# Optimization experiments

Measured on AMD Instinct MI355X. Metric: run time of the kernel, lower is better.

## Reference

```python
import jax, jax.numpy as jnp
import numpy as np

G, S, D, H, E = 8, 2048, 1024, 4096, 8  # groups, group_size, d_model, ffn_hidden, experts


def setup_inputs() -> dict:
    key = jax.random.key(0)
    ks = jax.random.split(key, 6)
    s = 0.02
    return {
        "x": jax.random.normal(ks[0], (G, S, D), dtype=jnp.float32),
        "gate_w": jax.random.normal(ks[1], (D, E), dtype=jnp.float32) * s,
        "ew1": jax.random.normal(ks[2], (E, D, H), dtype=jnp.float32) * s,
        "eb1": jnp.zeros((E, H), dtype=jnp.float32),
        "ew2": jax.random.normal(ks[3], (E, H, D), dtype=jnp.float32) * s,
        "eb2": jnp.zeros((E, D), dtype=jnp.float32),
        "sw1": jax.random.normal(ks[4], (D, H), dtype=jnp.float32) * s,
        "sb1": jnp.zeros((H,), dtype=jnp.float32),
        "sw2": jax.random.normal(ks[5], (H, D), dtype=jnp.float32) * s,
        "sb2": jnp.zeros((D,), dtype=jnp.float32),
        "expert_capacity": 2048,
    }


def reference(x, gate_w, ew1, eb1, ew2, eb2, sw1, sb1, sw2, sb2, expert_capacity):
    g, s_, d = x.shape
    e = gate_w.shape[1]
    T = g * s_
    cap = int(expert_capacity)

    # ---- Router (inference path) ----
    router_logits = jnp.einsum('gsd,de->gse', x, gate_w)           # (G,S,E)
    router_probs = jax.nn.softmax(router_logits, axis=-1)
    flat_probs = router_probs.transpose(2, 0, 1).reshape(e, T)      # (E,T)
    pad_w = max(0, cap - T)
    if pad_w > 0:
        flat_probs = jnp.pad(flat_probs, ((0, 0), (0, pad_w)),
                             mode='constant', constant_values=-1e9)
    scores, token_indices = jax.lax.top_k(flat_probs, k=cap)        # (E,C)
    scores = jnp.where(scores > -1e8, scores, 0.0)

    # ---- Routed experts: gather -> grouped FFN -> scale -> scatter-add ----
    x_flat = x.reshape(T, d)                                        # (T,D)
    safe_idx = jnp.clip(token_indices, 0, T - 1)                    # guard padded slots
    toks = x_flat[safe_idx]                                         # (E,C,D)
    h = jax.nn.gelu(jnp.einsum('ecd,edh->ech', toks, ew1) + eb1[:, None, :])
    y = jnp.einsum('ech,ehd->ecd', h, ew2) + eb2[:, None, :]        # (E,C,D)
    y = y * scores[..., None]                                       # zero weight kills padded slots
    routed = jnp.zeros_like(x_flat).at[safe_idx.reshape(-1)].add(y.reshape(-1, d))

    # ---- Shared expert over all tokens ----
    shared = jax.nn.gelu(x_flat @ sw1 + sb1) @ sw2 + sb2            # (T,D)

    return (routed + shared).reshape(g, s_, d)
```

## Files before the change

### kernel.cpp

```cpp
#include <hip/hip_runtime.h>

typedef __bf16 bf16;
typedef __bf16 bf16x8 __attribute__((ext_vector_type(8)));
typedef float f32x4 __attribute__((ext_vector_type(4)));

#define NTOK 16384
#define DMODEL 1024
#define HFFN 4096
#define NEXP 8
#define CAP 2048

#define VMCNT(n) asm volatile("s_waitcnt vmcnt(" #n ")" ::: "memory")
#define LGKM0() do { asm volatile("s_waitcnt lgkmcnt(0)" ::: "memory"); \
                     __builtin_amdgcn_sched_barrier(0); } while (0)
#define RAWBAR() do { __builtin_amdgcn_sched_barrier(0); \
                      __builtin_amdgcn_s_barrier(); \
                      __builtin_amdgcn_sched_barrier(0); } while (0)

__device__ __forceinline__ void gload16(const void* g, void* l) {
  __builtin_amdgcn_global_load_lds((const __attribute__((address_space(1))) void*)g,
                                   (__attribute__((address_space(3))) void*)l, 16, 0, 0);
}

__device__ __forceinline__ float gelu_f(float v) {
  float u = 0.7978845608028654f * (v + 0.044715f * v * v * v);
  float ex = __expf(2.0f * u);
  float th = 1.0f - 2.0f / (ex + 1.0f);
  return 0.5f * v * (1.0f + th);
}

__device__ __forceinline__ void xcd_remap(int& bx, int& by) {
  const int gx = gridDim.x;
  const int lg = 31 - __clz((unsigned)gx);
  const int w = blockIdx.x + gx * blockIdx.y;
  bx = (w >> 3) & (gx - 1);
  by = (w & 7) | (((w >> 3) >> lg) << 3);
}

__global__ __launch_bounds__(256) void cvt_x_kernel(const float* __restrict__ x,
                                                    bf16* __restrict__ xb) {
  int i = blockIdx.x * blockDim.x + threadIdx.x;
  const float4* a = (const float4*)x + (size_t)i * 2;
  float4 v0 = a[0], v1 = a[1];
  bf16x8 o;
  o[0]=(bf16)v0.x; o[1]=(bf16)v0.y; o[2]=(bf16)v0.z; o[3]=(bf16)v0.w;
  o[4]=(bf16)v1.x; o[5]=(bf16)v1.y; o[6]=(bf16)v1.z; o[7]=(bf16)v1.w;
  *(bf16x8*)(xb + (size_t)i * 8) = o;
}

__global__ __launch_bounds__(64) void router_kernel(const float* __restrict__ x,
                                                    const float* __restrict__ gw,
                                                    float* __restrict__ probs) {
  int t = blockIdx.x;
  int l = threadIdx.x;
  int e = l & 7, chunk = l >> 3;
  const float* xr = x + (size_t)t * DMODEL + chunk * 128;
  const float* gwr = gw + (size_t)(chunk * 128) * NEXP + e;
  float a0 = 0.f, a1 = 0.f;
  #pragma unroll
  for (int d = 0; d < 128; d += 8) {
    float4 xv = *(const float4*)(xr + d);
    float4 xw = *(const float4*)(xr + d + 4);
    a0 += xv.x * gwr[(d+0)*8] + xv.y * gwr[(d+1)*8] + xv.z * gwr[(d+2)*8] + xv.w * gwr[(d+3)*8];
    a1 += xw.x * gwr[(d+4)*8] + xw.y * gwr[(d+5)*8] + xw.z * gwr[(d+6)*8] + xw.w * gwr[(d+7)*8];
  }
  float acc = a0 + a1;
  acc += __shfl_xor(acc, 8);
  acc += __shfl_xor(acc, 16);
  acc += __shfl_xor(acc, 32);
  float m = acc;
  m = fmaxf(m, __shfl_xor(m, 1));
  m = fmaxf(m, __shfl_xor(m, 2));
  m = fmaxf(m, __shfl_xor(m, 4));
  float ex = expf(acc - m);
  float s = ex;
  s += __shfl_xor(s, 1); s += __shfl_xor(s, 2); s += __shfl_xor(s, 4);
  if (l < 8) probs[(size_t)e * NTOK + t] = ex / s;
}

__global__ __launch_bounds__(256) void topk_kernel(const float* __restrict__ probs,
                                                   int* __restrict__ oidx,
                                                   float* __restrict__ oscr) {
  const int e = blockIdx.x;
  const float* p = probs + (size_t)e * NTOK;
  const int t = threadIdx.x;
  __shared__ unsigned hist[256];
  __shared__ unsigned sg[256], sq[256];
  __shared__ unsigned bcast[4];
  unsigned pref = 0, krem = CAP;
  for (int pass = 0; pass < 4; ++pass) {
    const int sh = 24 - pass * 8;
    hist[t] = 0;
    __syncthreads();
    for (int j = 0; j < 64; ++j) {
      unsigned u = __float_as_uint(p[t * 64 + j]);
      bool ok = (pass == 0) || ((u >> (sh + 8)) == pref);
      if (ok) atomicAdd(&hist[(u >> sh) & 255u], 1u);
    }
    __syncthreads();
    if (t == 0) {
      unsigned cum = 0; int b = 255;
      for (; b > 0; --b) {
        unsigned c = hist[b];
        if (cum + c >= krem) break;
        cum += c;
      }
      bcast[0] = (pref << 8) | (unsigned)b;
      bcast[1] = krem - cum;
    }
    __syncthreads();
    pref = bcast[0];
    krem = bcast[1];
  }
  const unsigned thr = pref;
  const unsigned neq_take = krem;
  unsigned cgt = 0, ceq = 0;
  for (int j = 0; j < 64; ++j) {
    unsigned u = __float_as_uint(p[t * 64 + j]);
    cgt += (u > thr);
    ceq += (u == thr);
  }
  sg[t] = cgt; sq[t] = ceq;
  __syncthreads();
  if (t == 0) {
    unsigned ag = 0, aq = 0;
    for (int i = 0; i < 256; ++i) {
      unsigned g = sg[i], q = sq[i];
      sg[i] = ag; sq[i] = aq;
      ag += g; aq += q;
    }
    bcast[2] = ag;
  }
  __syncthreads();
  const unsigned ngt = bcast[2];
  unsigned og = sg[t], oq = sq[t];
  int* oi = oidx + e * CAP;
  float* os = oscr + e * CAP;
  for (int j = 0; j < 64; ++j) {
    int tok = t * 64 + j;
    float pv = p[tok];
    unsigned u = __float_as_uint(pv);
    if (u > thr) {
      oi[og] = tok; os[og] = pv; ++og;
    } else if (u == thr) {
      if (oq < neq_take) { oi[ngt + oq] = tok; os[ngt + oq] = pv; }
      ++oq;
    }
  }
}

__global__ __launch_bounds__(256) void transpose_cvt(const float* __restrict__ in_e,
                                                     const float* __restrict__ in_s,
                                                     bf16* __restrict__ outp,
                                                     int R, int C) {
  int z = blockIdx.z;
  const float* in = (z < 8) ? (in_e + (size_t)z * (size_t)R * C) : in_s;
  bf16* out = outp + (size_t)z * (size_t)R * C;
  __shared__ float tile[64][65];
  int tx = threadIdx.x & 63, ty = threadIdx.x >> 6;
  int c0 = blockIdx.x * 64, r0 = blockIdx.y * 64;
  #pragma unroll
  for (int j = 0; j < 16; ++j) {
    int r = ty + j * 4;
    tile[r][tx] = in[(size_t)(r0 + r) * C + c0 + tx];
  }
  __syncthreads();
  #pragma unroll
  for (int j = 0; j < 16; ++j) {
    int c = ty + j * 4;
    out[(size_t)(c0 + c) * R + r0 + tx] = (bf16)tile[tx][c];
  }
}


#define STAGE_TILE_ALL(tt) do { \
  bf16* D_ = smem + (((tt) & 1) << 15); \
  const int ko_ = (tt) * 64; \
  gload16(srcA0 + ko_, D_ + tid8); \
  gload16(srcA1 + ko_, D_ + 4096 + tid8); \
  gload16(srcA2 + ko_, D_ + 8192 + tid8); \
  gload16(srcA3 + ko_, D_ + 12288 + tid8); \
  gload16(srcB0 + ko_, D_ + 16384 + tid8); \
  gload16(srcB1 + ko_, D_ + 20480 + tid8); \
  gload16(srcB2 + ko_, D_ + 24576 + tid8); \
  gload16(srcB3 + ko_, D_ + 28672 + tid8); \
} while (0)

#define KLOOP8(NT) do { \
  STAGE_TILE_ALL(0); \
  STAGE_TILE_ALL(1); \
  VMCNT(8); \
  RAWBAR(); \
  for (int t = 0; t < (NT); ++t) { \
    const bf16* Ab_ = smem + ((t & 1) << 15); \
    const bf16* Bb_ = Ab_ + 16384; \
    bf16* Sn_ = smem + ((t & 1) << 15); \
    const int ko2 = (t + 2) * 64; \
    const bool st = (t + 2) < (NT); \
    bf16x8 aA[8], aB[8]; \
     \
    _Pragma("unroll") for (int i = 0; i < 4; ++i) { \
      aA[i*2+0] = *(const bf16x8*)(Ab_ + (wr*128 + i*16 + fr)*64 + c0s); \
      aA[i*2+1] = *(const bf16x8*)(Ab_ + (wr*128 + i*16 + fr)*64 + c1s); \
    } \
    _Pragma("unroll") for (int j = 0; j < 2; ++j) { \
      aB[j*2+0] = *(const bf16x8*)(Bb_ + (wc*64 + j*16 + fr)*64 + c0s); \
      aB[j*2+1] = *(const bf16x8*)(Bb_ + (wc*64 + j*16 + fr)*64 + c1s); \
    } \
    RAWBAR(); LGKM0(); \
    __builtin_amdgcn_s_setprio(1); \
    _Pragma("unroll") for (int i = 0; i < 4; ++i) \
      _Pragma("unroll") for (int j = 0; j < 2; ++j) { \
        acc[i][j] = __builtin_amdgcn_mfma_f32_16x16x32_bf16(aA[i*2+0], aB[j*2+0], acc[i][j], 0, 0, 0); \
        acc[i][j] = __builtin_amdgcn_mfma_f32_16x16x32_bf16(aA[i*2+1], aB[j*2+1], acc[i][j], 0, 0, 0); \
      } \
    __builtin_amdgcn_s_setprio(0); \
    RAWBAR(); \
     \
    _Pragma("unroll") for (int j = 0; j < 2; ++j) { \
      aB[4+j*2+0] = *(const bf16x8*)(Bb_ + (wc*64 + 32 + j*16 + fr)*64 + c0s); \
      aB[4+j*2+1] = *(const bf16x8*)(Bb_ + (wc*64 + 32 + j*16 + fr)*64 + c1s); \
    } \
    if (st) { \
      gload16(srcA0 + ko2, Sn_ + tid8); \
      gload16(srcA2 + ko2, Sn_ + 8192 + tid8); \
    } \
    RAWBAR(); LGKM0(); \
    __builtin_amdgcn_s_setprio(1); \
    _Pragma("unroll") for (int i = 0; i < 4; ++i) \
      _Pragma("unroll") for (int j = 0; j < 2; ++j) { \
        acc[i][2+j] = __builtin_amdgcn_mfma_f32_16x16x32_bf16(aA[i*2+0], aB[4+j*2+0], acc[i][2+j], 0, 0, 0); \
        acc[i][2+j] = __builtin_amdgcn_mfma_f32_16x16x32_bf16(aA[i*2+1], aB[4+j*2+1], acc[i][2+j], 0, 0, 0); \
      } \
    __builtin_amdgcn_s_setprio(0); \
    RAWBAR(); \
     \
    _Pragma("unroll") for (int i = 0; i < 4; ++i) { \
      aA[i*2+0] = *(const bf16x8*)(Ab_ + (wr*128 + 64 + i*16 + fr)*64 + c0s); \
      aA[i*2+1] = *(const bf16x8*)(Ab_ + (wr*128 + 64 + i*16 + fr)*64 + c1s); \
    } \
    if (st) { \
      gload16(srcB0 + ko2, Sn_ + 16384 + tid8); \
      gload16(srcB1 + ko2, Sn_ + 20480 + tid8); \
      gload16(srcB2 + ko2, Sn_ + 24576 + tid8); \
      gload16(srcB3 + ko2, Sn_ + 28672 + tid8); \
    } \
    RAWBAR(); LGKM0(); \
    __builtin_amdgcn_s_setprio(1); \
    _Pragma("unroll") for (int i = 0; i < 4; ++i) \
      _Pragma("unroll") for (int j = 0; j < 2; ++j) { \
        acc[4+i][j] = __builtin_amdgcn_mfma_f32_16x16x32_bf16(aA[i*2+0], aB[j*2+0], acc[4+i][j], 0, 0, 0); \
        acc[4+i][j] = __builtin_amdgcn_mfma_f32_16x16x32_bf16(aA[i*2+1], aB[j*2+1], acc[4+i][j], 0, 0, 0); \
      } \
    __builtin_amdgcn_s_setprio(0); \
    RAWBAR(); \
     \
    if (st) { \
      gload16(srcA1 + ko2, Sn_ + 4096 + tid8); \
      gload16(srcA3 + ko2, Sn_ + 12288 + tid8); \
    } \
    __builtin_amdgcn_s_setprio(1); \
    _Pragma("unroll") for (int i = 0; i < 4; ++i) \
      _Pragma("unroll") for (int j = 0; j < 2; ++j) { \
        acc[4+i][2+j] = __builtin_amdgcn_mfma_f32_16x16x32_bf16(aA[i*2+0], aB[4+j*2+0], acc[4+i][2+j], 0, 0, 0); \
        acc[4+i][2+j] = __builtin_amdgcn_mfma_f32_16x16x32_bf16(aA[i*2+1], aB[4+j*2+1], acc[4+i][2+j], 0, 0, 0); \
      } \
    __builtin_amdgcn_s_setprio(0); \
    if (st) { VMCNT(8); } else { VMCNT(0); } \
    RAWBAR(); \
  } \
} while (0)

__global__ __launch_bounds__(512, 2) void ffn1_gemm(const bf16* __restrict__ xb,
                                                    const bf16* __restrict__ w1t,
                                                    const float* __restrict__ bias1,
                                                    const int* __restrict__ sel,
                                                    bf16* __restrict__ hout,
                                                    int routed) {
  const int e = blockIdx.z;
  const bf16* Bw = w1t + (routed ? (size_t)e * HFFN * DMODEL : 0);
  const float* bias = bias1 + (routed ? (size_t)e * HFFN : 0);
  bf16* hb = hout + (routed ? (size_t)e * CAP * HFFN : 0);
  int bx, by;
  xcd_remap(bx, by);
  const int m0 = by * 256, n0 = bx * 256;
  __shared__ __align__(16) bf16 smem[65536];
  const int tid = threadIdx.x, lane = tid & 63, wave = tid >> 6;
  const int wr = wave >> 2, wc = wave & 3;
  const int tid8 = tid * 8;

  const int srow = tid >> 3, sch = tid & 7;
  const int schs = sch ^ (srow & 7);
  const bf16 *srcA0, *srcA1, *srcA2, *srcA3, *srcB0, *srcB1, *srcB2, *srcB3;
  {
    int ra0 = routed ? sel[e * CAP + m0 + srow]       : (m0 + srow);
    int ra1 = routed ? sel[e * CAP + m0 + 64 + srow]  : (m0 + 64 + srow);
    int ra2 = routed ? sel[e * CAP + m0 + 128 + srow] : (m0 + 128 + srow);
    int ra3 = routed ? sel[e * CAP + m0 + 192 + srow] : (m0 + 192 + srow);
    srcA0 = xb + (size_t)ra0 * DMODEL + schs * 8;
    srcA1 = xb + (size_t)ra1 * DMODEL + schs * 8;
    srcA2 = xb + (size_t)ra2 * DMODEL + schs * 8;
    srcA3 = xb + (size_t)ra3 * DMODEL + schs * 8;
    srcB0 = Bw + (size_t)(n0 + srow) * DMODEL + schs * 8;
    srcB1 = Bw + (size_t)(n0 + 64 + srow) * DMODEL + schs * 8;
    srcB2 = Bw + (size_t)(n0 + 128 + srow) * DMODEL + schs * 8;
    srcB3 = Bw + (size_t)(n0 + 192 + srow) * DMODEL + schs * 8;
  }

  f32x4 acc[8][4];
  #pragma unroll
  for (int i = 0; i < 8; ++i)
    #pragma unroll
    for (int j = 0; j < 4; ++j) acc[i][j] = (f32x4){0.f, 0.f, 0.f, 0.f};

  const int fr = lane & 15;
  const int k8 = lane >> 4;
  const int sw = lane & 7;
  const int c0s = (k8 ^ sw) * 8;
  const int c1s = ((k8 + 4) ^ sw) * 8;

  KLOOP8(DMODEL / 64);

  #pragma unroll
  for (int half = 0; half < 2; ++half) {
    if (wr == half) {
      #pragma unroll
      for (int i = 0; i < 8; ++i) {
        #pragma unroll
        for (int j = 0; j < 4; ++j) {
          const int nl = wc * 64 + j * 16 + fr;
          const float bb = bias[n0 + nl];
          #pragma unroll
          for (int q = 0; q < 4; ++q) {
            const int ml = i * 16 + (lane >> 4) * 4 + q;
            smem[ml * 256 + (nl ^ (((ml >> 2) & 7) << 4))] =
                (bf16)gelu_f(acc[i][j][q] + bb);
          }
        }
      }
    }
    __syncthreads();
    #pragma unroll
    for (int p = 0; p < 8; ++p) {
      const int flat = p * 512 + tid;
      const int row = flat >> 5, nc8 = flat & 31;
      uint4 v = *(const uint4*)(smem + row * 256 + ((nc8 * 8) ^ (((row >> 2) & 7) << 4)));
      *(uint4*)(hb + (size_t)(m0 + half * 128 + row) * HFFN + n0 + nc8 * 8) = v;
    }
    __syncthreads();
  }
}

__global__ __launch_bounds__(512, 2) void ffn2_gemm(const bf16* __restrict__ hbuf,
                                                    const bf16* __restrict__ w2t,
                                                    const float* __restrict__ bias2,
                                                    const int* __restrict__ sel,
                                                    const float* __restrict__ scr,
                                                    float* __restrict__ out,
                                                    int routed) {
  const int e = blockIdx.z;
  const bf16* Ab = hbuf + (routed ? (size_t)e * CAP * HFFN : 0);
  const bf16* Bw = w2t + (routed ? (size_t)e * DMODEL * HFFN : 0);
  const float* bias = bias2 + (routed ? (size_t)e * DMODEL : 0);
  int bx, by;
  xcd_remap(bx, by);
  const int m0 = by * 256, n0 = bx * 256;
  __shared__ __align__(16) bf16 smem[65536];
  __shared__ int s_tok[256];
  __shared__ float s_scl[256];
  const int tid = threadIdx.x, lane = tid & 63, wave = tid >> 6;
  const int wr = wave >> 2, wc = wave & 3;
  const int tid8 = tid * 8;

  const int srow = tid >> 3, sch = tid & 7;
  const int schs = sch ^ (srow & 7);
  const bf16* srcA0 = Ab + (size_t)(m0 + srow) * HFFN + schs * 8;
  const bf16* srcA1 = Ab + (size_t)(m0 + 64 + srow) * HFFN + schs * 8;
  const bf16* srcA2 = Ab + (size_t)(m0 + 128 + srow) * HFFN + schs * 8;
  const bf16* srcA3 = Ab + (size_t)(m0 + 192 + srow) * HFFN + schs * 8;
  const bf16* srcB0 = Bw + (size_t)(n0 + srow) * HFFN + schs * 8;
  const bf16* srcB1 = Bw + (size_t)(n0 + 64 + srow) * HFFN + schs * 8;
  const bf16* srcB2 = Bw + (size_t)(n0 + 128 + srow) * HFFN + schs * 8;
  const bf16* srcB3 = Bw + (size_t)(n0 + 192 + srow) * HFFN + schs * 8;
  if (routed && tid < 256) {
    s_tok[tid] = sel[e * CAP + m0 + tid];
    s_scl[tid] = scr[e * CAP + m0 + tid];
  }

  f32x4 acc[8][4];
  #pragma unroll
  for (int i = 0; i < 8; ++i)
    #pragma unroll
    for (int j = 0; j < 4; ++j) acc[i][j] = (f32x4){0.f, 0.f, 0.f, 0.f};

  const int fr = lane & 15;
  const int k8 = lane >> 4;
  const int sw = lane & 7;
  const int c0s = (k8 ^ sw) * 8;
  const int c1s = ((k8 + 4) ^ sw) * 8;

  KLOOP8(HFFN / 64);

  if (!routed) {
    #pragma unroll
    for (int i = 0; i < 8; ++i) {
      #pragma unroll
      for (int j = 0; j < 4; ++j) {
        const int nl = wc * 64 + j * 16 + fr;
        const float bb = bias[n0 + nl];
        #pragma unroll
        for (int q = 0; q < 4; ++q) {
          const int ml = wr * 128 + i * 16 + (lane >> 4) * 4 + q;
          out[(size_t)(m0 + ml) * DMODEL + n0 + nl] = acc[i][j][q] + bb;
        }
      }
    }
  } else {
    __syncthreads();
    #pragma unroll
    for (int i = 0; i < 8; ++i) {
      #pragma unroll
      for (int j = 0; j < 4; ++j) {
        const int nl = wc * 64 + j * 16 + fr;
        const float bb = bias[n0 + nl];
        #pragma unroll
        for (int q = 0; q < 4; ++q) {
          const int ml = wr * 128 + i * 16 + (lane >> 4) * 4 + q;
          const int tok = s_tok[ml];
          const float sc = s_scl[ml];
          atomicAdd(out + (size_t)tok * DMODEL + n0 + nl, (acc[i][j][q] + bb) * sc);
        }
      }
    }
  }
}

extern "C" void kernel_launch(void* const* d_in, const int* in_sizes, int n_in,
                              void* d_out, int out_size, void* d_ws, size_t ws_size,
                              hipStream_t stream) {
  const float* x   = (const float*)d_in[0];
  const float* gw  = (const float*)d_in[1];
  const float* ew1 = (const float*)d_in[2];
  const float* eb1 = (const float*)d_in[3];
  const float* ew2 = (const float*)d_in[4];
  const float* eb2 = (const float*)d_in[5];
  const float* sw1 = (const float*)d_in[6];
  const float* sb1 = (const float*)d_in[7];
  const float* sw2 = (const float*)d_in[8];
  const float* sb2 = (const float*)d_in[9];
  float* out = (float*)d_out;

  char* ws = (char*)d_ws;
  size_t off = 0;
  bf16* xb      = (bf16*)(ws + off); off += (size_t)NTOK * DMODEL * 2;
  bf16* w1t     = (bf16*)(ws + off); off += (size_t)9 * HFFN * DMODEL * 2;
  bf16* w2t     = (bf16*)(ws + off); off += (size_t)9 * DMODEL * HFFN * 2;
  bf16* hbuf    = (bf16*)(ws + off); off += (size_t)NTOK * HFFN * 2;
  float* probs  = (float*)(ws + off); off += (size_t)NEXP * NTOK * 4;
  int* selidx   = (int*)(ws + off);   off += (size_t)NEXP * CAP * 4;
  float* selscr = (float*)(ws + off); off += (size_t)NEXP * CAP * 4;

  cvt_x_kernel<<<dim3(NTOK * DMODEL / 8 / 256), dim3(256), 0, stream>>>(x, xb);
  router_kernel<<<dim3(NTOK), dim3(64), 0, stream>>>(x, gw, probs);
  topk_kernel<<<dim3(NEXP), dim3(256), 0, stream>>>(probs, selidx, selscr);
  transpose_cvt<<<dim3(HFFN / 64, DMODEL / 64, 9), dim3(256), 0, stream>>>(ew1, sw1, w1t, DMODEL, HFFN);
  transpose_cvt<<<dim3(DMODEL / 64, HFFN / 64, 9), dim3(256), 0, stream>>>(ew2, sw2, w2t, HFFN, DMODEL);

  ffn1_gemm<<<dim3(HFFN / 256, NTOK / 256, 1), dim3(512), 0, stream>>>(
      xb, w1t + (size_t)8 * HFFN * DMODEL, sb1, (const int*)nullptr, hbuf, 0);
  ffn2_gemm<<<dim3(DMODEL / 256, NTOK / 256, 1), dim3(512), 0, stream>>>(
      hbuf, w2t + (size_t)8 * DMODEL * HFFN, sb2, (const int*)nullptr, (const float*)nullptr, out, 0);

  ffn1_gemm<<<dim3(HFFN / 256, CAP / 256, NEXP), dim3(512), 0, stream>>>(
      xb, w1t, eb1, selidx, hbuf, 1);
  ffn2_gemm<<<dim3(DMODEL / 256, CAP / 256, NEXP), dim3(512), 0, stream>>>(
      hbuf, w2t, eb2, selidx, selscr, out, 1);
}
```

Measured before the change: 897.2 us.

## Rework GEMM K-loop prefetch schedule with fewer barriers and cheaper GELU

Restructures the double-buffered K-loop so the A1/A3 halves of the next tile load one step earlier, and the remaining loads for tile t+2 go into the current buffer after it has been consumed. This removes the sched_barrier fences around s_barrier and cuts the barriers per iteration from eight to four, with the vmcnt wait moved before the last MFMA group. GELU's tanh form is also rewritten as a sigmoid using exp2 and a hardware reciprocal to shorten the epilogue. The reordered buffer reuse risks LDS read/write races if the barrier placement is wrong, and removing the sched_barriers lets the compiler move loads across barriers.

New measurement: 821.3 us. 8.5% less time.

```diff
diff --git a/kernel.cpp b/kernel.cpp
--- a/kernel.cpp
+++ b/kernel.cpp
@@ -13,9 +13,7 @@
 #define VMCNT(n) asm volatile("s_waitcnt vmcnt(" #n ")" ::: "memory")
 #define LGKM0() do { asm volatile("s_waitcnt lgkmcnt(0)" ::: "memory"); \
                      __builtin_amdgcn_sched_barrier(0); } while (0)
-#define RAWBAR() do { __builtin_amdgcn_sched_barrier(0); \
-                      __builtin_amdgcn_s_barrier(); \
-                      __builtin_amdgcn_sched_barrier(0); } while (0)
+#define BARRIER() __builtin_amdgcn_s_barrier()
 
 __device__ __forceinline__ void gload16(const void* g, void* l) {
   __builtin_amdgcn_global_load_lds((const __attribute__((address_space(1))) void*)g,
@@ -23,10 +21,10 @@
 }
 
 __device__ __forceinline__ float gelu_f(float v) {
-  float u = 0.7978845608028654f * (v + 0.044715f * v * v * v);
-  float ex = __expf(2.0f * u);
-  float th = 1.0f - 2.0f / (ex + 1.0f);
-  return 0.5f * v * (1.0f + th);
+  float t = v * v;
+  float s2 = v * fmaf(0.10294358f, t, 2.3022084f);
+  float e = __builtin_exp2f(-s2);
+  return v * __builtin_amdgcn_rcpf(1.0f + e);
 }
 
 __device__ __forceinline__ void xcd_remap(int& bx, int& by) {
@@ -188,15 +186,24 @@
 
 #define KLOOP8(NT) do { \
   STAGE_TILE_ALL(0); \
-  STAGE_TILE_ALL(1); \
-  VMCNT(8); \
-  RAWBAR(); \
+  {  \
+    bf16* D_ = smem + 32768; \
+    gload16(srcA0 + 64, D_ + tid8); \
+    gload16(srcA2 + 64, D_ + 8192 + tid8); \
+    gload16(srcB0 + 64, D_ + 16384 + tid8); \
+    gload16(srcB1 + 64, D_ + 20480 + tid8); \
+    gload16(srcB2 + 64, D_ + 24576 + tid8); \
+    gload16(srcB3 + 64, D_ + 28672 + tid8); \
+  } \
+  VMCNT(6); \
+  BARRIER(); \
   for (int t = 0; t < (NT); ++t) { \
     const bf16* Ab_ = smem + ((t & 1) << 15); \
     const bf16* Bb_ = Ab_ + 16384; \
-    bf16* Sn_ = smem + ((t & 1) << 15); \
-    const int ko2 = (t + 2) * 64; \
-    const bool st = (t + 2) < (NT); \
+    bf16* Scur = smem + ((t & 1) << 15); \
+    bf16* Snxt = smem + (((t + 1) & 1) << 15); \
+    const int ko1 = (t + 1) * 64, ko2 = (t + 2) * 64; \
+    const bool st1 = (t + 1) < (NT), st2 = (t + 2) < (NT); \
     bf16x8 aA[8], aB[8]; \
      \
     _Pragma("unroll") for (int i = 0; i < 4; ++i) { \
@@ -207,7 +214,11 @@
       aB[j*2+0] = *(const bf16x8*)(Bb_ + (wc*64 + j*16 + fr)*64 + c0s); \
       aB[j*2+1] = *(const bf16x8*)(Bb_ + (wc*64 + j*16 + fr)*64 + c1s); \
     } \
-    RAWBAR(); LGKM0(); \
+    if (st1) { \
+      gload16(srcA1 + ko1, Snxt + 4096 + tid8); \
+      gload16(srcA3 + ko1, Snxt + 12288 + tid8); \
+    } \
+    BARRIER(); LGKM0(); \
     __builtin_amdgcn_s_setprio(1); \
     _Pragma("unroll") for (int i = 0; i < 4; ++i) \
       _Pragma("unroll") for (int j = 0; j < 2; ++j) { \
@@ -215,17 +226,12 @@
         acc[i][j] = __builtin_amdgcn_mfma_f32_16x16x32_bf16(aA[i*2+1], aB[j*2+1], acc[i][j], 0, 0, 0); \
       } \
     __builtin_amdgcn_s_setprio(0); \
-    RAWBAR(); \
      \
     _Pragma("unroll") for (int j = 0; j < 2; ++j) { \
       aB[4+j*2+0] = *(const bf16x8*)(Bb_ + (wc*64 + 32 + j*16 + fr)*64 + c0s); \
       aB[4+j*2+1] = *(const bf16x8*)(Bb_ + (wc*64 + 32 + j*16 + fr)*64 + c1s); \
     } \
-    if (st) { \
-      gload16(srcA0 + ko2, Sn_ + tid8); \
-      gload16(srcA2 + ko2, Sn_ + 8192 + tid8); \
-    } \
-    RAWBAR(); LGKM0(); \
+    BARRIER(); LGKM0(); \
     __builtin_amdgcn_s_setprio(1); \
     _Pragma("unroll") for (int i = 0; i < 4; ++i) \
       _Pragma("unroll") for (int j = 0; j < 2; ++j) { \
@@ -233,19 +239,16 @@
         acc[i][2+j] = __builtin_amdgcn_mfma_f32_16x16x32_bf16(aA[i*2+1], aB[4+j*2+1], acc[i][2+j], 0, 0, 0); \
       } \
     __builtin_amdgcn_s_setprio(0); \
-    RAWBAR(); \
      \
     _Pragma("unroll") for (int i = 0; i < 4; ++i) { \
       aA[i*2+0] = *(const bf16x8*)(Ab_ + (wr*128 + 64 + i*16 + fr)*64 + c0s); \
       aA[i*2+1] = *(const bf16x8*)(Ab_ + (wr*128 + 64 + i*16 + fr)*64 + c1s); \
     } \
-    if (st) { \
-      gload16(srcB0 + ko2, Sn_ + 16384 + tid8); \
-      gload16(srcB1 + ko2, Sn_ + 20480 + tid8); \
-      gload16(srcB2 + ko2, Sn_ + 24576 + tid8); \
-      gload16(srcB3 + ko2, Sn_ + 28672 + tid8); \
-    } \
-    RAWBAR(); LGKM0(); \
+    if (st2) { \
+      gload16(srcA0 + ko2, Scur + tid8); \
+      gload16(srcA2 + ko2, Scur + 8192 + tid8); \
+    } \
+    BARRIER(); LGKM0(); \
     __builtin_amdgcn_s_setprio(1); \
     _Pragma("unroll") for (int i = 0; i < 4; ++i) \
       _Pragma("unroll") for (int j = 0; j < 2; ++j) { \
@@ -253,12 +256,15 @@
         acc[4+i][j] = __builtin_amdgcn_mfma_f32_16x16x32_bf16(aA[i*2+1], aB[j*2+1], acc[4+i][j], 0, 0, 0); \
       } \
     __builtin_amdgcn_s_setprio(0); \
-    RAWBAR(); \
      \
-    if (st) { \
-      gload16(srcA1 + ko2, Sn_ + 4096 + tid8); \
-      gload16(srcA3 + ko2, Sn_ + 12288 + tid8); \
-    } \
+    if (st2) { \
+      gload16(srcB0 + ko2, Scur + 16384 + tid8); \
+      gload16(srcB1 + ko2, Scur + 20480 + tid8); \
+      gload16(srcB2 + ko2, Scur + 24576 + tid8); \
+      gload16(srcB3 + ko2, Scur + 28672 + tid8); \
+    } \
+    if (st2) { VMCNT(6); } else { VMCNT(0); } \
+    BARRIER(); \
     __builtin_amdgcn_s_setprio(1); \
     _Pragma("unroll") for (int i = 0; i < 4; ++i) \
       _Pragma("unroll") for (int j = 0; j < 2; ++j) { \
@@ -266,8 +272,6 @@
         acc[4+i][2+j] = __builtin_amdgcn_mfma_f32_16x16x32_bf16(aA[i*2+1], aB[4+j*2+1], acc[4+i][2+j], 0, 0, 0); \
       } \
     __builtin_amdgcn_s_setprio(0); \
-    if (st) { VMCNT(8); } else { VMCNT(0); } \
-    RAWBAR(); \
   } \
 } while (0)
 
@@ -321,6 +325,7 @@
 
   KLOOP8(DMODEL / 64);
 
+  __syncthreads();
   #pragma unroll
   for (int half = 0; half < 2; ++half) {
     if (wr == half) {
```
